# Optimization experiments

Hardware: AMD Instinct MI355X
Metric: run time of the kernel (lower is better)

## Reference

```python
import jax, jax.numpy as jnp
import numpy as np

B, T, C, H = 2, 2048, 1024, 16
D = C // H  # head_dim = 64


def setup_inputs() -> dict:
    key = jax.random.key(0)
    ks = jax.random.split(key, 12)
    s = 1.0 / np.sqrt(C)
    inp = {
        "q": jax.random.normal(ks[0], (B, T, C), jnp.float32),
        "k": jax.random.normal(ks[1], (B, T, C), jnp.float32),
        "v": jax.random.normal(ks[2], (B, T, C), jnp.float32),
        "mask": jnp.tril(jnp.ones((T, T), jnp.int32)),  # causal mask; 0 = masked
        "Wq": jax.random.normal(ks[3], (C, C), jnp.float32) * s,
        "bq": jax.random.normal(ks[4], (C,), jnp.float32) * s,
        "Wk": jax.random.normal(ks[5], (C, C), jnp.float32) * s,
        "bk": jax.random.normal(ks[6], (C,), jnp.float32) * s,
        "Wv": jax.random.normal(ks[7], (C, C), jnp.float32) * s,
        "bv": jax.random.normal(ks[8], (C,), jnp.float32) * s,
        "Wo": jax.random.normal(ks[9], (C, C), jnp.float32) * s,
        "bo": jax.random.normal(ks[10], (C,), jnp.float32) * s,
    }
    return inp


def reference(q, k, v, mask, Wq, bq, Wk, bk, Wv, bv, Wo, bo):
    # Linear projections (torch Linear: x @ W.T + b)
    qh = (q @ Wq.T + bq).reshape(B, T, H, D).transpose(0, 2, 1, 3)  # [B,H,T,D]
    kh = (k @ Wk.T + bk).reshape(B, -1, H, D).transpose(0, 2, 1, 3)
    vh = (v @ Wv.T + bv).reshape(B, -1, H, D).transpose(0, 2, 1, 3)
    scores = jnp.einsum("bhtd,bhsd->bhts", qh, kh) / jnp.sqrt(jnp.float32(D))
    scores = jnp.where(mask[None, None, :, :] == 0, -jnp.inf, scores)
    attn = jax.nn.softmax(scores, axis=-1)
    out = jnp.einsum("bhts,bhsd->bhtd", attn, vh)  # [B,H,T,D]
    out = out.transpose(0, 2, 1, 3).reshape(B, T, C)
    return out @ Wo.T + bo
```

## Files before the change

### kernel.cpp

```cpp
#include <hip/hip_runtime.h>
#include <hip/hip_bf16.h>

#define BB 2
#define TT 2048
#define CC 1024
#define HH 16
#define DD 64
#define MM (BB * TT)

typedef __bf16 bf16;
typedef __bf16 bf16x4 __attribute__((ext_vector_type(4)));
typedef __bf16 bf16x8 __attribute__((ext_vector_type(8)));
typedef float f32x4 __attribute__((ext_vector_type(4)));

__device__ __forceinline__ void gload16(const bf16* g, bf16* l) {
    __builtin_amdgcn_global_load_lds(
        (__attribute__((address_space(1))) void*)g,
        (__attribute__((address_space(3))) void*)l, 16, 0, 0);
}

__global__ __launch_bounds__(256) void to_bf16(
    const float* __restrict__ q, const float* __restrict__ k,
    const float* __restrict__ v,
    const float* __restrict__ wq, const float* __restrict__ wk,
    const float* __restrict__ wv, const float* __restrict__ wo,
    bf16* __restrict__ xq, bf16* __restrict__ xk, bf16* __restrict__ xv,
    bf16* __restrict__ owq, bf16* __restrict__ owk, bf16* __restrict__ owv,
    bf16* __restrict__ owo)
{
    const unsigned XE = 1u << 22;
    const unsigned WE = 1u << 20;
    const unsigned NC = (3u * XE + 4u * WE) >> 3;
    for (unsigned c = blockIdx.x * blockDim.x + threadIdx.x; c < NC;
         c += gridDim.x * blockDim.x) {
        const unsigned e = c << 3;
        const float* src; bf16* dst; unsigned off;
        if (e < 3u * XE) {
            const unsigned t = e >> 22; off = e & (XE - 1u);
            src = (t == 0) ? q : (t == 1) ? k : v;
            dst = (t == 0) ? xq : (t == 1) ? xk : xv;
        } else {
            const unsigned e2 = e - 3u * XE;
            const unsigned t = e2 >> 20; off = e2 & (WE - 1u);
            src = (t == 0) ? wq : (t == 1) ? wk : (t == 2) ? wv : wo;
            dst = (t == 0) ? owq : (t == 1) ? owk : (t == 2) ? owv : owo;
        }
        const f32x4 a = *reinterpret_cast<const f32x4*>(src + off);
        const f32x4 b = *reinterpret_cast<const f32x4*>(src + off + 4);
        bf16x8 r;
#pragma unroll
        for (int j = 0; j < 4; ++j) { r[j] = (bf16)a[j]; r[j + 4] = (bf16)b[j]; }
        *reinterpret_cast<bf16x8*>(dst + off) = r;
    }
}

template <typename TOUT, int HEAD_LAYOUT>
__device__ __forceinline__ void gemm_tile_body(
    const bf16* __restrict__ X, const bf16* __restrict__ W,
    const float* __restrict__ bias, TOUT* __restrict__ out,
    bf16* lA, bf16* lB, int vmode)
{
    const int tid  = threadIdx.x;
    const int lane = tid & 63;
    const int quad = lane >> 4;
    const int lm   = lane & 15;
    const int wave = tid >> 6;
    const int m0 = blockIdx.x << 7;
    const int n0 = blockIdx.y << 7;
    const int wrow = (wave >> 1) << 6;
    const int wcol = (wave & 1) << 6;

    const int c0 = tid, c1 = tid + 256;
    const bf16* gA0 = X + (size_t)(m0 + (c0 >> 2)) * CC + (c0 & 3) * 8;
    const bf16* gA1 = X + (size_t)(m0 + (c1 >> 2)) * CC + (c1 & 3) * 8;
    const bf16* gB0 = W + (size_t)(n0 + (c0 >> 2)) * CC + (c0 & 3) * 8;
    const bf16* gB1 = W + (size_t)(n0 + (c1 >> 2)) * CC + (c1 & 3) * 8;
    bf16* lAw0 = lA + wave * 512;
    bf16* lAw1 = lA + 2048 + wave * 512;
    bf16* lBw0 = lB + wave * 512;
    bf16* lBw1 = lB + 2048 + wave * 512;

    f32x4 acc[4][4];
#pragma unroll
    for (int i = 0; i < 4; ++i)
#pragma unroll
        for (int j = 0; j < 4; ++j) acc[i][j] = (f32x4){0.f, 0.f, 0.f, 0.f};

    for (int kk = 0; kk < CC; kk += 32) {
        __syncthreads();
        gload16(gA0 + kk, lAw0);
        gload16(gA1 + kk, lAw1);
        gload16(gB0 + kk, lBw0);
        gload16(gB1 + kk, lBw1);
        __syncthreads();

        bf16x8 af[4], bf_[4];
#pragma unroll
        for (int i = 0; i < 4; ++i)
            af[i] = *reinterpret_cast<const bf16x8*>(
                lA + (wrow + i * 16 + lm) * 32 + quad * 8);
#pragma unroll
        for (int j = 0; j < 4; ++j)
            bf_[j] = *reinterpret_cast<const bf16x8*>(
                lB + (wcol + j * 16 + lm) * 32 + quad * 8);
#pragma unroll
        for (int i = 0; i < 4; ++i)
#pragma unroll
            for (int j = 0; j < 4; ++j)
                acc[i][j] = __builtin_amdgcn_mfma_f32_16x16x32_bf16(
                    af[i], bf_[j], acc[i][j], 0, 0, 0);
    }

#pragma unroll
    for (int j = 0; j < 4; ++j) {
        const int col = n0 + wcol + j * 16 + lm;
        const float bv = bias[col];
        if (vmode) {
            const int h = col / DD, d = col % DD;
#pragma unroll
            for (int i = 0; i < 4; ++i) {
                const int m = m0 + wrow + i * 16 + quad * 4;
                const int b_ = m / TT, t = m % TT;
                bf16x4 o;
#pragma unroll
                for (int r = 0; r < 4; ++r) o[r] = (bf16)(acc[i][j][r] + bv);
                *reinterpret_cast<bf16x4*>(
                    (bf16*)out + (((size_t)(b_ * HH + h)) * DD + d) * TT + t) = o;
            }
        } else {
#pragma unroll
            for (int i = 0; i < 4; ++i)
#pragma unroll
                for (int r = 0; r < 4; ++r) {
                    const int m = m0 + wrow + i * 16 + quad * 4 + r;
                    const float v = acc[i][j][r] + bv;
                    if (HEAD_LAYOUT) {
                        const int b_ = m / TT, t = m % TT;
                        const int h = col / DD, d = col % DD;
                        out[(((size_t)(b_ * HH + h)) * TT + t) * DD + d] = (TOUT)v;
                    } else {
                        out[(size_t)m * CC + col] = (TOUT)v;
                    }
                }
        }
    }
}

__global__ __launch_bounds__(256) void gemm_qkv(
    const bf16* __restrict__ x0, const bf16* __restrict__ x1,
    const bf16* __restrict__ x2,
    const bf16* __restrict__ w0, const bf16* __restrict__ w1,
    const bf16* __restrict__ w2,
    const float* __restrict__ b0, const float* __restrict__ b1,
    const float* __restrict__ b2,
    bf16* __restrict__ o0, bf16* __restrict__ o1, bf16* __restrict__ o2)
{
    __shared__ __align__(16) bf16 lA[128 * 32];
    __shared__ __align__(16) bf16 lB[128 * 32];
    const int z = blockIdx.z;
    const bf16* X = (z == 0) ? x0 : (z == 1) ? x1 : x2;
    const bf16* W = (z == 0) ? w0 : (z == 1) ? w1 : w2;
    const float* bias = (z == 0) ? b0 : (z == 1) ? b1 : b2;
    bf16* out = (z == 0) ? o0 : (z == 1) ? o1 : o2;
    gemm_tile_body<bf16, 1>(X, W, bias, out, lA, lB, (z == 2) ? 1 : 0);
}

__global__ __launch_bounds__(256) void gemm_oproj(
    const bf16* __restrict__ X, const bf16* __restrict__ W,
    const float* __restrict__ bias, float* __restrict__ out)
{
    __shared__ __align__(16) bf16 lA[128 * 32];
    __shared__ __align__(16) bf16 lB[128 * 32];
    gemm_tile_body<float, 0>(X, W, bias, out, lA, lB, 0);
}

__device__ __forceinline__ void issue_k(const bf16* __restrict__ Kh,
                                        size_t baseQK, int s0, int kKey,
                                        int kDc, bf16x8* kreg) {
#pragma unroll
    for (int it = 0; it < 2; ++it)
        kreg[it] = *reinterpret_cast<const bf16x8*>(
            Kh + baseQK + (size_t)(s0 + kKey + it * 32) * DD + kDc * 8);
}
__device__ __forceinline__ void issue_v(const bf16* __restrict__ Vt,
                                        size_t baseVT, int s0, int vD,
                                        int vSc, bf16x8* vreg) {
#pragma unroll
    for (int it = 0; it < 2; ++it)
        vreg[it] = *reinterpret_cast<const bf16x8*>(
            Vt + baseVT + (size_t)vD * TT + s0 + (vSc + it * 4) * 8);
}
__device__ __forceinline__ void write_k(bf16* buf, int kKey, int kDc,
                                        const bf16x8* kreg) {
#pragma unroll
    for (int it = 0; it < 2; ++it)
        *reinterpret_cast<bf16x8*>(&buf[(kKey + it * 32) * 72 + kDc * 8]) =
            kreg[it];
}
__device__ __forceinline__ void write_v(bf16* buf, int vD, int vSc,
                                        const bf16x8* vreg) {
#pragma unroll
    for (int it = 0; it < 2; ++it) {
        const int sc = vSc + it * 4;
        const int c2 = sc >> 2, h = (sc >> 1) & 1, q0 = (sc & 1) * 2;
        bf16x4 lo, hi;
#pragma unroll
        for (int j = 0; j < 4; ++j) { lo[j] = vreg[it][j]; hi[j] = vreg[it][4 + j]; }
        *reinterpret_cast<bf16x4*>(
            &buf[((c2 * 4 + q0) * 64 + vD) * 8 + h * 4]) = lo;
        *reinterpret_cast<bf16x4*>(
            &buf[((c2 * 4 + q0 + 1) * 64 + vD) * 8 + h * 4]) = hi;
    }
}
__device__ __forceinline__ void qk_tile(const bf16* bufK, int lm, int koff,
                                        bf16x8 qf0, bf16x8 qf1,
                                        float sv[4][4]) {
#pragma unroll
    for (int st = 0; st < 4; ++st) {
        const bf16* kp = &bufK[(st * 16 + lm) * 72 + koff];
        bf16x8 k0 = *reinterpret_cast<const bf16x8*>(kp);
        bf16x8 k1 = *reinterpret_cast<const bf16x8*>(kp + 32);
        f32x4 s = {0.f, 0.f, 0.f, 0.f};
        s = __builtin_amdgcn_mfma_f32_16x16x32_bf16(k0, qf0, s, 0, 0, 0);
        s = __builtin_amdgcn_mfma_f32_16x16x32_bf16(k1, qf1, s, 0, 0, 0);
#pragma unroll
        for (int r = 0; r < 4; ++r) sv[st][r] = s[r];
    }
}
__device__ __forceinline__ float tmax4(const float s[4]) {
    return fmaxf(fmaxf(s[0], s[1]), fmaxf(s[2], s[3]));
}

__global__ __launch_bounds__(256) void attn_fused(
    const bf16* __restrict__ Qh, const bf16* __restrict__ Kh,
    const bf16* __restrict__ Vt, bf16* __restrict__ attn_out)
{
    __shared__ __align__(16) bf16 ldsK[4][64 * 72];
    __shared__ __align__(16) bf16 ldsV[4][8 * 64 * 8];

    const int tid  = threadIdx.x;
    const int lane = tid & 63;
    const int wave = tid >> 6;
    const int xp = blockIdx.x;
    const int bh = blockIdx.y;
    const int b_ = bh >> 4, h = bh & 15;
    const size_t baseQK = (size_t)bh * TT * DD;
    const size_t baseVT = (size_t)bh * DD * TT;
    const int lm   = lane & 15;
    const int quad = lane >> 4;
    const int koff = quad * 8;

    const int kKey = tid >> 3, kDc = tid & 7;
    const int vD   = tid >> 2, vSc = tid & 3;

    for (int pass = 0; pass < 2; ++pass) {
        const int qb = pass == 0 ? (TT / 64 - 1 - xp) : xp;
        const int q0 = qb * 64 + wave * 16;
        const int q_lane = q0 + lm;
        const int ntiles = qb + 1;
        const int npairs = ntiles >> 1;
        const int has_tail = ntiles & 1;

        const bf16* qp = Qh + baseQK + (size_t)q_lane * DD + koff;
        bf16x8 qr0 = *reinterpret_cast<const bf16x8*>(qp);
        bf16x8 qr1 = *reinterpret_cast<const bf16x8*>(qp + 32);
        bf16x8 qf0, qf1;
#pragma unroll
        for (int j = 0; j < 8; ++j) {
            qf0[j] = (bf16)((float)qr0[j] * 0.125f);
            qf1[j] = (bf16)((float)qr1[j] * 0.125f);
        }

        f32x4 Oacc[4];
#pragma unroll
        for (int dt = 0; dt < 4; ++dt) Oacc[dt] = (f32x4){0.f, 0.f, 0.f, 0.f};
        float m_run = -1e30f, l_run = 0.f;

        bf16x8 kregA[2], vregA[2], kregB[2], vregB[2];
        issue_k(Kh, baseQK, 0, kKey, kDc, kregA);
        issue_v(Vt, baseVT, 0, vD, vSc, vregA);
        if (ntiles > 1) {
            issue_k(Kh, baseQK, 64, kKey, kDc, kregB);
            issue_v(Vt, baseVT, 64, vD, vSc, vregB);
        }
        __syncthreads();

        int base = 0;
        for (int j = 0; j < npairs; ++j) {
            const int t1 = 2 * j + 1;

            write_k(ldsK[base], kKey, kDc, kregA);
            write_v(ldsV[base], vD, vSc, vregA);
            write_k(ldsK[base + 1], kKey, kDc, kregB);
            write_v(ldsV[base + 1], vD, vSc, vregB);
            __syncthreads();

            if (t1 + 1 < ntiles) {
                issue_k(Kh, baseQK, (t1 + 1) * 64, kKey, kDc, kregA);
                issue_v(Vt, baseVT, (t1 + 1) * 64, vD, vSc, vregA);
            }
            if (t1 + 2 < ntiles) {
                issue_k(Kh, baseQK, (t1 + 2) * 64, kKey, kDc, kregB);
                issue_v(Vt, baseVT, (t1 + 2) * 64, vD, vSc, vregB);
            }

            float svA[4][4], svB[4][4];
            __builtin_amdgcn_s_setprio(1);
            qk_tile(ldsK[base], lm, koff, qf0, qf1, svA);
            qk_tile(ldsK[base + 1], lm, koff, qf0, qf1, svB);
            __builtin_amdgcn_s_setprio(0);

            if (t1 == qb) {
                const int s0b = t1 * 64;
#pragma unroll
                for (int st = 0; st < 4; ++st) {
                    const int kbase = s0b + st * 16 + quad * 4;
#pragma unroll
                    for (int r = 0; r < 4; ++r)
                        if (kbase + r > q_lane) svB[st][r] = -1e30f;
                }
            }

            float rm[8];
#pragma unroll
            for (int st = 0; st < 4; ++st) { rm[st] = tmax4(svA[st]); rm[4 + st] = tmax4(svB[st]); }
            float mx = fmaxf(
                fmaxf(fmaxf(rm[0], rm[1]), fmaxf(rm[2], rm[3])),
                fmaxf(fmaxf(rm[4], rm[5]), fmaxf(rm[6], rm[7])));
            mx = fmaxf(mx, __shfl_xor(mx, 16));
            mx = fmaxf(mx, __shfl_xor(mx, 32));
            if (__any(mx > m_run)) {
                const float mn = fmaxf(m_run, mx);
                const float alpha = __expf(m_run - mn);
                m_run = mn;
                l_run *= alpha;
#pragma unroll
                for (int dt = 0; dt < 4; ++dt) Oacc[dt] *= alpha;
            }
            float ps[8];
#pragma unroll
            for (int st = 0; st < 4; ++st) {
                float p0 = __expf(svA[st][0] - m_run);
                float p1 = __expf(svA[st][1] - m_run);
                float p2 = __expf(svA[st][2] - m_run);
                float p3 = __expf(svA[st][3] - m_run);
                svA[st][0] = p0; svA[st][1] = p1; svA[st][2] = p2; svA[st][3] = p3;
                ps[st] = (p0 + p1) + (p2 + p3);
                float b0 = __expf(svB[st][0] - m_run);
                float b1 = __expf(svB[st][1] - m_run);
                float b2 = __expf(svB[st][2] - m_run);
                float b3 = __expf(svB[st][3] - m_run);
                svB[st][0] = b0; svB[st][1] = b1; svB[st][2] = b2; svB[st][3] = b3;
                ps[4 + st] = (b0 + b1) + (b2 + b3);
            }
            float srow = ((ps[0] + ps[1]) + (ps[2] + ps[3]))
                       + ((ps[4] + ps[5]) + (ps[6] + ps[7]));
            srow += __shfl_xor(srow, 16);
            srow += __shfl_xor(srow, 32);
            l_run += srow;

            bf16x8 pf[4];
#pragma unroll
            for (int c = 0; c < 2; ++c)
#pragma unroll
                for (int jj = 0; jj < 4; ++jj) {
                    pf[c][jj]         = (bf16)svA[2 * c][jj];
                    pf[c][4 + jj]     = (bf16)svA[2 * c + 1][jj];
                    pf[2 + c][jj]     = (bf16)svB[2 * c][jj];
                    pf[2 + c][4 + jj] = (bf16)svB[2 * c + 1][jj];
                }

            __builtin_amdgcn_s_setprio(1);
#pragma unroll
            for (int dt = 0; dt < 4; ++dt) {
                const int d = dt * 16 + lm;
#pragma unroll
                for (int c = 0; c < 4; ++c) {
                    const bf16* vp = &ldsV[base + (c >> 1)]
                        [(((c & 1) * 4 + quad) * 64 + d) * 8];
                    bf16x8 vf = *reinterpret_cast<const bf16x8*>(vp);
                    Oacc[dt] = __builtin_amdgcn_mfma_f32_16x16x32_bf16(
                        vf, pf[c], Oacc[dt], 0, 0, 0);
                }
            }
            __builtin_amdgcn_s_setprio(0);
            base ^= 2;
        }

        if (has_tail) {
            write_k(ldsK[base], kKey, kDc, kregA);
            write_v(ldsV[base], vD, vSc, vregA);
            __syncthreads();

            float sv[4][4];
            __builtin_amdgcn_s_setprio(1);
            qk_tile(ldsK[base], lm, koff, qf0, qf1, sv);
            __builtin_amdgcn_s_setprio(0);
            const int s0 = qb * 64;
#pragma unroll
            for (int st = 0; st < 4; ++st) {
                const int kbase = s0 + st * 16 + quad * 4;
#pragma unroll
                for (int r = 0; r < 4; ++r)
                    if (kbase + r > q_lane) sv[st][r] = -1e30f;
            }
            float rm[4];
#pragma unroll
            for (int st = 0; st < 4; ++st) rm[st] = tmax4(sv[st]);
            float mx = fmaxf(fmaxf(rm[0], rm[1]), fmaxf(rm[2], rm[3]));
            mx = fmaxf(mx, __shfl_xor(mx, 16));
            mx = fmaxf(mx, __shfl_xor(mx, 32));
            if (__any(mx > m_run)) {
                const float mn = fmaxf(m_run, mx);
                const float alpha = __expf(m_run - mn);
                m_run = mn;
                l_run *= alpha;
#pragma unroll
                for (int dt = 0; dt < 4; ++dt) Oacc[dt] *= alpha;
            }
            float ps[4];
#pragma unroll
            for (int st = 0; st < 4; ++st) {
                float p0 = __expf(sv[st][0] - m_run);
                float p1 = __expf(sv[st][1] - m_run);
                float p2 = __expf(sv[st][2] - m_run);
                float p3 = __expf(sv[st][3] - m_run);
                sv[st][0] = p0; sv[st][1] = p1; sv[st][2] = p2; sv[st][3] = p3;
                ps[st] = (p0 + p1) + (p2 + p3);
            }
            float srow = (ps[0] + ps[1]) + (ps[2] + ps[3]);
            srow += __shfl_xor(srow, 16);
            srow += __shfl_xor(srow, 32);
            l_run += srow;

            bf16x8 pf[2];
#pragma unroll
            for (int c = 0; c < 2; ++c)
#pragma unroll
                for (int jj = 0; jj < 4; ++jj) {
                    pf[c][jj]     = (bf16)sv[2 * c][jj];
                    pf[c][4 + jj] = (bf16)sv[2 * c + 1][jj];
                }
            __builtin_amdgcn_s_setprio(1);
#pragma unroll
            for (int dt = 0; dt < 4; ++dt) {
                const int d = dt * 16 + lm;
#pragma unroll
                for (int c = 0; c < 2; ++c) {
                    const bf16* vp = &ldsV[base][((c * 4 + quad) * 64 + d) * 8];
                    bf16x8 vf = *reinterpret_cast<const bf16x8*>(vp);
                    Oacc[dt] = __builtin_amdgcn_mfma_f32_16x16x32_bf16(
                        vf, pf[c], Oacc[dt], 0, 0, 0);
                }
            }
            __builtin_amdgcn_s_setprio(0);
        }

        const float inv_l = 1.0f / l_run;
        bf16* dst = attn_out + ((size_t)(b_ * TT + q_lane)) * CC + h * DD;
#pragma unroll
        for (int dt = 0; dt < 4; ++dt) {
            bf16x4 o;
#pragma unroll
            for (int r = 0; r < 4; ++r) o[r] = (bf16)(Oacc[dt][r] * inv_l);
            *reinterpret_cast<bf16x4*>(dst + dt * 16 + quad * 4) = o;
        }
    }
}

extern "C" void kernel_launch(void* const* d_in, const int* in_sizes, int n_in,
                              void* d_out, int out_size, void* d_ws,
                              size_t ws_size, hipStream_t stream)
{
    const float* q  = (const float*)d_in[0];
    const float* k  = (const float*)d_in[1];
    const float* v  = (const float*)d_in[2];
    const float* Wq = (const float*)d_in[4];
    const float* bq = (const float*)d_in[5];
    const float* Wk = (const float*)d_in[6];
    const float* bk = (const float*)d_in[7];
    const float* Wv = (const float*)d_in[8];
    const float* bv = (const float*)d_in[9];
    const float* Wo = (const float*)d_in[10];
    const float* bo = (const float*)d_in[11];
    float* out = (float*)d_out;

    bf16* Qh   = (bf16*)d_ws;
    bf16* Kh   = Qh + (size_t)MM * CC;
    bf16* Vt   = Kh + (size_t)MM * CC;
    bf16* attn = Vt + (size_t)MM * CC;
    bf16* Xq   = attn + (size_t)MM * CC;
    bf16* Xk   = Xq + (size_t)MM * CC;
    bf16* Xv   = Xk + (size_t)MM * CC;
    bf16* Wqb  = Xv + (size_t)MM * CC;
    bf16* Wkb  = Wqb + (size_t)CC * CC;
    bf16* Wvb  = Wkb + (size_t)CC * CC;
    bf16* Wob  = Wvb + (size_t)CC * CC;

    const dim3 blk(256);
    to_bf16<<<dim3(2048), blk, 0, stream>>>(
        q, k, v, Wq, Wk, Wv, Wo, Xq, Xk, Xv, Wqb, Wkb, Wvb, Wob);
    gemm_qkv<<<dim3(MM / 128, CC / 128, 3), blk, 0, stream>>>(
        Xq, Xk, Xv, Wqb, Wkb, Wvb, bq, bk, bv, Qh, Kh, Vt);
    attn_fused<<<dim3(TT / 128, BB * HH), blk, 0, stream>>>(Qh, Kh, Vt, attn);
    gemm_oproj<<<dim3(MM / 128, CC / 128), blk, 0, stream>>>(
        attn, Wob, bo, out);
}
```

Baseline: 227.6 us.

## Split attention passes across grid z and shrink output-projection tile rows

The attention kernel no longer runs two causal passes per block. Each pass becomes its own block along grid z, which doubles the block count and halves the LDS buffers (4 to 2), so occupancy should rise. A trailing barrier is added per iteration to guard the single buffer pair. The output projection gets its own 64x128 tile GEMM, doubling its grid to fill more CUs, at the cost of less reuse of the weight tile.

After: 232.2 us. About the same (+2.0%).

```diff
diff --git a/kernel.cpp b/kernel.cpp
--- a/kernel.cpp
+++ b/kernel.cpp
@@ -169,9 +169,69 @@
     const bf16* __restrict__ X, const bf16* __restrict__ W,
     const float* __restrict__ bias, float* __restrict__ out)
 {
-    __shared__ __align__(16) bf16 lA[128 * 32];
+    __shared__ __align__(16) bf16 lA[64 * 32];
     __shared__ __align__(16) bf16 lB[128 * 32];
-    gemm_tile_body<float, 0>(X, W, bias, out, lA, lB, 0);
+    const int tid  = threadIdx.x;
+    const int lane = tid & 63;
+    const int quad = lane >> 4;
+    const int lm   = lane & 15;
+    const int wave = tid >> 6;
+    const int m0 = blockIdx.x << 6;
+    const int n0 = blockIdx.y << 7;
+    const int wrow = (wave >> 1) << 5;
+    const int wcol = (wave & 1) << 6;
+
+    const int cA = tid;
+    const int c0 = tid, c1 = tid + 256;
+    const bf16* gA0 = X + (size_t)(m0 + (cA >> 2)) * CC + (cA & 3) * 8;
+    const bf16* gB0 = W + (size_t)(n0 + (c0 >> 2)) * CC + (c0 & 3) * 8;
+    const bf16* gB1 = W + (size_t)(n0 + (c1 >> 2)) * CC + (c1 & 3) * 8;
+    bf16* lAw  = lA + wave * 512;
+    bf16* lBw0 = lB + wave * 512;
+    bf16* lBw1 = lB + 2048 + wave * 512;
+
+    f32x4 acc[2][4];
+#pragma unroll
+    for (int i = 0; i < 2; ++i)
+#pragma unroll
+        for (int j = 0; j < 4; ++j) acc[i][j] = (f32x4){0.f, 0.f, 0.f, 0.f};
+
+    for (int kk = 0; kk < CC; kk += 32) {
+        __syncthreads();
+        gload16(gA0 + kk, lAw);
+        gload16(gB0 + kk, lBw0);
+        gload16(gB1 + kk, lBw1);
+        __syncthreads();
+
+        bf16x8 af[2], bf_[4];
+#pragma unroll
+        for (int i = 0; i < 2; ++i)
+            af[i] = *reinterpret_cast<const bf16x8*>(
+                lA + (wrow + i * 16 + lm) * 32 + quad * 8);
+#pragma unroll
+        for (int j = 0; j < 4; ++j)
+            bf_[j] = *reinterpret_cast<const bf16x8*>(
+                lB + (wcol + j * 16 + lm) * 32 + quad * 8);
+#pragma unroll
+        for (int i = 0; i < 2; ++i)
+#pragma unroll
+            for (int j = 0; j < 4; ++j)
+                acc[i][j] = __builtin_amdgcn_mfma_f32_16x16x32_bf16(
+                    af[i], bf_[j], acc[i][j], 0, 0, 0);
+    }
+
+#pragma unroll
+    for (int j = 0; j < 4; ++j) {
+        const int col = n0 + wcol + j * 16 + lm;
+        const float bv = bias[col];
+#pragma unroll
+        for (int i = 0; i < 2; ++i)
+#pragma unroll
+            for (int r = 0; r < 4; ++r) {
+                const int m = m0 + wrow + i * 16 + quad * 4 + r;
+                out[(size_t)m * CC + col] = acc[i][j][r] + bv;
+            }
+    }
 }
 
 __device__ __forceinline__ void issue_k(const bf16* __restrict__ Kh,
@@ -235,8 +295,8 @@
     const bf16* __restrict__ Qh, const bf16* __restrict__ Kh,
     const bf16* __restrict__ Vt, bf16* __restrict__ attn_out)
 {
-    __shared__ __align__(16) bf16 ldsK[4][64 * 72];
-    __shared__ __align__(16) bf16 ldsV[4][8 * 64 * 8];
+    __shared__ __align__(16) bf16 ldsK[2][64 * 72];
+    __shared__ __align__(16) bf16 ldsV[2][8 * 64 * 8];
 
     const int tid  = threadIdx.x;
     const int lane = tid & 63;
@@ -253,218 +313,214 @@
     const int kKey = tid >> 3, kDc = tid & 7;
     const int vD   = tid >> 2, vSc = tid & 3;
 
-    for (int pass = 0; pass < 2; ++pass) {
-        const int qb = pass == 0 ? (TT / 64 - 1 - xp) : xp;
-        const int q0 = qb * 64 + wave * 16;
-        const int q_lane = q0 + lm;
-        const int ntiles = qb + 1;
-        const int npairs = ntiles >> 1;
-        const int has_tail = ntiles & 1;
-
-        const bf16* qp = Qh + baseQK + (size_t)q_lane * DD + koff;
-        bf16x8 qr0 = *reinterpret_cast<const bf16x8*>(qp);
-        bf16x8 qr1 = *reinterpret_cast<const bf16x8*>(qp + 32);
-        bf16x8 qf0, qf1;
-#pragma unroll
-        for (int j = 0; j < 8; ++j) {
-            qf0[j] = (bf16)((float)qr0[j] * 0.125f);
-            qf1[j] = (bf16)((float)qr1[j] * 0.125f);
-        }
-
-        f32x4 Oacc[4];
-#pragma unroll
-        for (int dt = 0; dt < 4; ++dt) Oacc[dt] = (f32x4){0.f, 0.f, 0.f, 0.f};
-        float m_run = -1e30f, l_run = 0.f;
-
-        bf16x8 kregA[2], vregA[2], kregB[2], vregB[2];
-        issue_k(Kh, baseQK, 0, kKey, kDc, kregA);
-        issue_v(Vt, baseVT, 0, vD, vSc, vregA);
-        if (ntiles > 1) {
-            issue_k(Kh, baseQK, 64, kKey, kDc, kregB);
-            issue_v(Vt, baseVT, 64, vD, vSc, vregB);
-        }
-        __syncthreads();
-
-        int base = 0;
-        for (int j = 0; j < npairs; ++j) {
-            const int t1 = 2 * j + 1;
-
-            write_k(ldsK[base], kKey, kDc, kregA);
-            write_v(ldsV[base], vD, vSc, vregA);
-            write_k(ldsK[base + 1], kKey, kDc, kregB);
-            write_v(ldsV[base + 1], vD, vSc, vregB);
-            __syncthreads();
-
-            if (t1 + 1 < ntiles) {
-                issue_k(Kh, baseQK, (t1 + 1) * 64, kKey, kDc, kregA);
-                issue_v(Vt, baseVT, (t1 + 1) * 64, vD, vSc, vregA);
-            }
-            if (t1 + 2 < ntiles) {
-                issue_k(Kh, baseQK, (t1 + 2) * 64, kKey, kDc, kregB);
-                issue_v(Vt, baseVT, (t1 + 2) * 64, vD, vSc, vregB);
-            }
-
-            float svA[4][4], svB[4][4];
-            __builtin_amdgcn_s_setprio(1);
-            qk_tile(ldsK[base], lm, koff, qf0, qf1, svA);
-            qk_tile(ldsK[base + 1], lm, koff, qf0, qf1, svB);
-            __builtin_amdgcn_s_setprio(0);
-
-            if (t1 == qb) {
-                const int s0b = t1 * 64;
-#pragma unroll
-                for (int st = 0; st < 4; ++st) {
-                    const int kbase = s0b + st * 16 + quad * 4;
-#pragma unroll
-                    for (int r = 0; r < 4; ++r)
-                        if (kbase + r > q_lane) svB[st][r] = -1e30f;
-                }
-            }
-
-            float rm[8];
-#pragma unroll
-            for (int st = 0; st < 4; ++st) { rm[st] = tmax4(svA[st]); rm[4 + st] = tmax4(svB[st]); }
-            float mx = fmaxf(
-                fmaxf(fmaxf(rm[0], rm[1]), fmaxf(rm[2], rm[3])),
-                fmaxf(fmaxf(rm[4], rm[5]), fmaxf(rm[6], rm[7])));
-            mx = fmaxf(mx, __shfl_xor(mx, 16));
-            mx = fmaxf(mx, __shfl_xor(mx, 32));
-            if (__any(mx > m_run)) {
-                const float mn = fmaxf(m_run, mx);
-                const float alpha = __expf(m_run - mn);
-                m_run = mn;
-                l_run *= alpha;
-#pragma unroll
-                for (int dt = 0; dt < 4; ++dt) Oacc[dt] *= alpha;
-            }
-            float ps[8];
+    const int qb = (blockIdx.z == 0) ? (TT / 64 - 1 - xp) : xp;
+    const int q0 = qb * 64 + wave * 16;
+    const int q_lane = q0 + lm;
+    const int ntiles = qb + 1;
+    const int npairs = ntiles >> 1;
+    const int has_tail = ntiles & 1;
+
+    const bf16* qp = Qh + baseQK + (size_t)q_lane * DD + koff;
+    bf16x8 qr0 = *reinterpret_cast<const bf16x8*>(qp);
+    bf16x8 qr1 = *reinterpret_cast<const bf16x8*>(qp + 32);
+    bf16x8 qf0, qf1;
+#pragma unroll
+    for (int j = 0; j < 8; ++j) {
+        qf0[j] = (bf16)((float)qr0[j] * 0.125f);
+        qf1[j] = (bf16)((float)qr1[j] * 0.125f);
+    }
+
+    f32x4 Oacc[4];
+#pragma unroll
+    for (int dt = 0; dt < 4; ++dt) Oacc[dt] = (f32x4){0.f, 0.f, 0.f, 0.f};
+    float m_run = -1e30f, l_run = 0.f;
+
+    bf16x8 kregA[2], vregA[2], kregB[2], vregB[2];
+    issue_k(Kh, baseQK, 0, kKey, kDc, kregA);
+    issue_v(Vt, baseVT, 0, vD, vSc, vregA);
+    if (ntiles > 1) {
+        issue_k(Kh, baseQK, 64, kKey, kDc, kregB);
+        issue_v(Vt, baseVT, 64, vD, vSc, vregB);
+    }
+
+    for (int j = 0; j < npairs; ++j) {
+        const int t1 = 2 * j + 1;
+
+        write_k(ldsK[0], kKey, kDc, kregA);
+        write_v(ldsV[0], vD, vSc, vregA);
+        write_k(ldsK[1], kKey, kDc, kregB);
+        write_v(ldsV[1], vD, vSc, vregB);
+        __syncthreads();
+
+        if (t1 + 1 < ntiles) {
+            issue_k(Kh, baseQK, (t1 + 1) * 64, kKey, kDc, kregA);
+            issue_v(Vt, baseVT, (t1 + 1) * 64, vD, vSc, vregA);
+        }
+        if (t1 + 2 < ntiles) {
+            issue_k(Kh, baseQK, (t1 + 2) * 64, kKey, kDc, kregB);
+            issue_v(Vt, baseVT, (t1 + 2) * 64, vD, vSc, vregB);
+        }
+
+        float svA[4][4], svB[4][4];
+        __builtin_amdgcn_s_setprio(1);
+        qk_tile(ldsK[0], lm, koff, qf0, qf1, svA);
+        qk_tile(ldsK[1], lm, koff, qf0, qf1, svB);
+        __builtin_amdgcn_s_setprio(0);
+
+        if (t1 == qb) {
+            const int s0b = t1 * 64;
 #pragma unroll
             for (int st = 0; st < 4; ++st) {
-                float p0 = __expf(svA[st][0] - m_run);
-                float p1 = __expf(svA[st][1] - m_run);
-                float p2 = __expf(svA[st][2] - m_run);
-                float p3 = __expf(svA[st][3] - m_run);
-                svA[st][0] = p0; svA[st][1] = p1; svA[st][2] = p2; svA[st][3] = p3;
-                ps[st] = (p0 + p1) + (p2 + p3);
-                float b0 = __expf(svB[st][0] - m_run);
-                float b1 = __expf(svB[st][1] - m_run);
-                float b2 = __expf(svB[st][2] - m_run);
-                float b3 = __expf(svB[st][3] - m_run);
-                svB[st][0] = b0; svB[st][1] = b1; svB[st][2] = b2; svB[st][3] = b3;
-                ps[4 + st] = (b0 + b1) + (b2 + b3);
-            }
-            float srow = ((ps[0] + ps[1]) + (ps[2] + ps[3]))
-                       + ((ps[4] + ps[5]) + (ps[6] + ps[7]));
-            srow += __shfl_xor(srow, 16);
-            srow += __shfl_xor(srow, 32);
-            l_run += srow;
-
-            bf16x8 pf[4];
-#pragma unroll
-            for (int c = 0; c < 2; ++c)
-#pragma unroll
-                for (int jj = 0; jj < 4; ++jj) {
-                    pf[c][jj]         = (bf16)svA[2 * c][jj];
-                    pf[c][4 + jj]     = (bf16)svA[2 * c + 1][jj];
-                    pf[2 + c][jj]     = (bf16)svB[2 * c][jj];
-                    pf[2 + c][4 + jj] = (bf16)svB[2 * c + 1][jj];
-                }
-
-            __builtin_amdgcn_s_setprio(1);
-#pragma unroll
-            for (int dt = 0; dt < 4; ++dt) {
-                const int d = dt * 16 + lm;
-#pragma unroll
-                for (int c = 0; c < 4; ++c) {
-                    const bf16* vp = &ldsV[base + (c >> 1)]
-                        [(((c & 1) * 4 + quad) * 64 + d) * 8];
-                    bf16x8 vf = *reinterpret_cast<const bf16x8*>(vp);
-                    Oacc[dt] = __builtin_amdgcn_mfma_f32_16x16x32_bf16(
-                        vf, pf[c], Oacc[dt], 0, 0, 0);
-                }
-            }
-            __builtin_amdgcn_s_setprio(0);
-            base ^= 2;
-        }
-
-        if (has_tail) {
-            write_k(ldsK[base], kKey, kDc, kregA);
-            write_v(ldsV[base], vD, vSc, vregA);
-            __syncthreads();
-
-            float sv[4][4];
-            __builtin_amdgcn_s_setprio(1);
-            qk_tile(ldsK[base], lm, koff, qf0, qf1, sv);
-            __builtin_amdgcn_s_setprio(0);
-            const int s0 = qb * 64;
-#pragma unroll
-            for (int st = 0; st < 4; ++st) {
-                const int kbase = s0 + st * 16 + quad * 4;
+                const int kbase = s0b + st * 16 + quad * 4;
 #pragma unroll
                 for (int r = 0; r < 4; ++r)
-                    if (kbase + r > q_lane) sv[st][r] = -1e30f;
-            }
-            float rm[4];
-#pragma unroll
-            for (int st = 0; st < 4; ++st) rm[st] = tmax4(sv[st]);
-            float mx = fmaxf(fmaxf(rm[0], rm[1]), fmaxf(rm[2], rm[3]));
-            mx = fmaxf(mx, __shfl_xor(mx, 16));
-            mx = fmaxf(mx, __shfl_xor(mx, 32));
-            if (__any(mx > m_run)) {
-                const float mn = fmaxf(m_run, mx);
-                const float alpha = __expf(m_run - mn);
-                m_run = mn;
-                l_run *= alpha;
-#pragma unroll
-                for (int dt = 0; dt < 4; ++dt) Oacc[dt] *= alpha;
-            }
-            float ps[4];
-#pragma unroll
-            for (int st = 0; st < 4; ++st) {
-                float p0 = __expf(sv[st][0] - m_run);
-                float p1 = __expf(sv[st][1] - m_run);
-                float p2 = __expf(sv[st][2] - m_run);
-                float p3 = __expf(sv[st][3] - m_run);
-                sv[st][0] = p0; sv[st][1] = p1; sv[st][2] = p2; sv[st][3] = p3;
-                ps[st] = (p0 + p1) + (p2 + p3);
-            }
-            float srow = (ps[0] + ps[1]) + (ps[2] + ps[3]);
-            srow += __shfl_xor(srow, 16);
-            srow += __shfl_xor(srow, 32);
-            l_run += srow;
-
-            bf16x8 pf[2];
-#pragma unroll
-            for (int c = 0; c < 2; ++c)
-#pragma unroll
-                for (int jj = 0; jj < 4; ++jj) {
-                    pf[c][jj]     = (bf16)sv[2 * c][jj];
-                    pf[c][4 + jj] = (bf16)sv[2 * c + 1][jj];
-                }
-            __builtin_amdgcn_s_setprio(1);
-#pragma unroll
-            for (int dt = 0; dt < 4; ++dt) {
-                const int d = dt * 16 + lm;
-#pragma unroll
-                for (int c = 0; c < 2; ++c) {
-                    const bf16* vp = &ldsV[base][((c * 4 + quad) * 64 + d) * 8];
-                    bf16x8 vf = *reinterpret_cast<const bf16x8*>(vp);
-                    Oacc[dt] = __builtin_amdgcn_mfma_f32_16x16x32_bf16(
-                        vf, pf[c], Oacc[dt], 0, 0, 0);
-                }
-            }
-            __builtin_amdgcn_s_setprio(0);
-        }
-
-        const float inv_l = 1.0f / l_run;
-        bf16* dst = attn_out + ((size_t)(b_ * TT + q_lane)) * CC + h * DD;
+                    if (kbase + r > q_lane) svB[st][r] = -1e30f;
+            }
+        }
+
+        float rm[8];
+#pragma unroll
+        for (int st = 0; st < 4; ++st) { rm[st] = tmax4(svA[st]); rm[4 + st] = tmax4(svB[st]); }
+        float mx = fmaxf(
+            fmaxf(fmaxf(rm[0], rm[1]), fmaxf(rm[2], rm[3])),
+            fmaxf(fmaxf(rm[4], rm[5]), fmaxf(rm[6], rm[7])));
+        mx = fmaxf(mx, __shfl_xor(mx, 16));
+        mx = fmaxf(mx, __shfl_xor(mx, 32));
+        if (__any(mx > m_run)) {
+            const float mn = fmaxf(m_run, mx);
+            const float alpha = __expf(m_run - mn);
+            m_run = mn;
+            l_run *= alpha;
+#pragma unroll
+            for (int dt = 0; dt < 4; ++dt) Oacc[dt] *= alpha;
+        }
+        float ps[8];
+#pragma unroll
+        for (int st = 0; st < 4; ++st) {
+            float p0 = __expf(svA[st][0] - m_run);
+            float p1 = __expf(svA[st][1] - m_run);
+            float p2 = __expf(svA[st][2] - m_run);
+            float p3 = __expf(svA[st][3] - m_run);
+            svA[st][0] = p0; svA[st][1] = p1; svA[st][2] = p2; svA[st][3] = p3;
+            ps[st] = (p0 + p1) + (p2 + p3);
+            float b0 = __expf(svB[st][0] - m_run);
+            float b1 = __expf(svB[st][1] - m_run);
+            float b2 = __expf(svB[st][2] - m_run);
+            float b3 = __expf(svB[st][3] - m_run);
+            svB[st][0] = b0; svB[st][1] = b1; svB[st][2] = b2; svB[st][3] = b3;
+            ps[4 + st] = (b0 + b1) + (b2 + b3);
+        }
+        float srow = ((ps[0] + ps[1]) + (ps[2] + ps[3]))
+                   + ((ps[4] + ps[5]) + (ps[6] + ps[7]));
+        srow += __shfl_xor(srow, 16);
+        srow += __shfl_xor(srow, 32);
+        l_run += srow;
+
+        bf16x8 pf[4];
+#pragma unroll
+        for (int c = 0; c < 2; ++c)
+#pragma unroll
+            for (int jj = 0; jj < 4; ++jj) {
+                pf[c][jj]         = (bf16)svA[2 * c][jj];
+                pf[c][4 + jj]     = (bf16)svA[2 * c + 1][jj];
+                pf[2 + c][jj]     = (bf16)svB[2 * c][jj];
+                pf[2 + c][4 + jj] = (bf16)svB[2 * c + 1][jj];
+            }
+
+        __builtin_amdgcn_s_setprio(1);
 #pragma unroll
         for (int dt = 0; dt < 4; ++dt) {
-            bf16x4 o;
-#pragma unroll
-            for (int r = 0; r < 4; ++r) o[r] = (bf16)(Oacc[dt][r] * inv_l);
-            *reinterpret_cast<bf16x4*>(dst + dt * 16 + quad * 4) = o;
-        }
+            const int d = dt * 16 + lm;
+#pragma unroll
+            for (int c = 0; c < 4; ++c) {
+                const bf16* vp = &ldsV[c >> 1]
+                    [(((c & 1) * 4 + quad) * 64 + d) * 8];
+                bf16x8 vf = *reinterpret_cast<const bf16x8*>(vp);
+                Oacc[dt] = __builtin_amdgcn_mfma_f32_16x16x32_bf16(
+                    vf, pf[c], Oacc[dt], 0, 0, 0);
+            }
+        }
+        __builtin_amdgcn_s_setprio(0);
+        __syncthreads();
+    }
+
+    if (has_tail) {
+        write_k(ldsK[0], kKey, kDc, kregA);
+        write_v(ldsV[0], vD, vSc, vregA);
+        __syncthreads();
+
+        float sv[4][4];
+        __builtin_amdgcn_s_setprio(1);
+        qk_tile(ldsK[0], lm, koff, qf0, qf1, sv);
+        __builtin_amdgcn_s_setprio(0);
+        const int s0 = qb * 64;
+#pragma unroll
+        for (int st = 0; st < 4; ++st) {
+            const int kbase = s0 + st * 16 + quad * 4;
+#pragma unroll
+            for (int r = 0; r < 4; ++r)
+                if (kbase + r > q_lane) sv[st][r] = -1e30f;
+        }
+        float rm[4];
+#pragma unroll
+        for (int st = 0; st < 4; ++st) rm[st] = tmax4(sv[st]);
+        float mx = fmaxf(fmaxf(rm[0], rm[1]), fmaxf(rm[2], rm[3]));
+        mx = fmaxf(mx, __shfl_xor(mx, 16));
+        mx = fmaxf(mx, __shfl_xor(mx, 32));
+        if (__any(mx > m_run)) {
+            const float mn = fmaxf(m_run, mx);
+            const float alpha = __expf(m_run - mn);
+            m_run = mn;
+            l_run *= alpha;
+#pragma unroll
+            for (int dt = 0; dt < 4; ++dt) Oacc[dt] *= alpha;
+        }
+        float ps[4];
+#pragma unroll
+        for (int st = 0; st < 4; ++st) {
+            float p0 = __expf(sv[st][0] - m_run);
+            float p1 = __expf(sv[st][1] - m_run);
+            float p2 = __expf(sv[st][2] - m_run);
+            float p3 = __expf(sv[st][3] - m_run);
+            sv[st][0] = p0; sv[st][1] = p1; sv[st][2] = p2; sv[st][3] = p3;
+            ps[st] = (p0 + p1) + (p2 + p3);
+        }
+        float srow = (ps[0] + ps[1]) + (ps[2] + ps[3]);
+        srow += __shfl_xor(srow, 16);
+        srow += __shfl_xor(srow, 32);
+        l_run += srow;
+
+        bf16x8 pf[2];
+#pragma unroll
+        for (int c = 0; c < 2; ++c)
+#pragma unroll
+            for (int jj = 0; jj < 4; ++jj) {
+                pf[c][jj]     = (bf16)sv[2 * c][jj];
+                pf[c][4 + jj] = (bf16)sv[2 * c + 1][jj];
+            }
+        __builtin_amdgcn_s_setprio(1);
+#pragma unroll
+        for (int dt = 0; dt < 4; ++dt) {
+            const int d = dt * 16 + lm;
+#pragma unroll
+            for (int c = 0; c < 2; ++c) {
+                const bf16* vp = &ldsV[0][((c * 4 + quad) * 64 + d) * 8];
+                bf16x8 vf = *reinterpret_cast<const bf16x8*>(vp);
+                Oacc[dt] = __builtin_amdgcn_mfma_f32_16x16x32_bf16(
+                    vf, pf[c], Oacc[dt], 0, 0, 0);
+            }
+        }
+        __builtin_amdgcn_s_setprio(0);
+    }
+
+    const float inv_l = 1.0f / l_run;
+    bf16* dst = attn_out + ((size_t)(b_ * TT + q_lane)) * CC + h * DD;
+#pragma unroll
+    for (int dt = 0; dt < 4; ++dt) {
+        bf16x4 o;
+#pragma unroll
+        for (int r = 0; r < 4; ++r) o[r] = (bf16)(Oacc[dt][r] * inv_l);
+        *reinterpret_cast<bf16x4*>(dst + dt * 16 + quad * 4) = o;
     }
 }
 
@@ -502,7 +558,8 @@
         q, k, v, Wq, Wk, Wv, Wo, Xq, Xk, Xv, Wqb, Wkb, Wvb, Wob);
     gemm_qkv<<<dim3(MM / 128, CC / 128, 3), blk, 0, stream>>>(
         Xq, Xk, Xv, Wqb, Wkb, Wvb, bq, bk, bv, Qh, Kh, Vt);
-    attn_fused<<<dim3(TT / 128, BB * HH), blk, 0, stream>>>(Qh, Kh, Vt, attn);
-    gemm_oproj<<<dim3(MM / 128, CC / 128), blk, 0, stream>>>(
+    attn_fused<<<dim3(TT / 128, BB * HH, 2), blk, 0, stream>>>(
+        Qh, Kh, Vt, attn);
+    gemm_oproj<<<dim3(MM / 64, CC / 128), blk, 0, stream>>>(
         attn, Wob, bo, out);
 }
```
